# Optimization experiments

Measured on AMD Instinct MI355X. Metric: run time of the kernel, lower is better.

## Reference

```python
import jax, jax.numpy as jnp
import numpy as np

BN_EPS = 1e-5


def three_nn(unknown, known):
    # squared pairwise distances via gemm form: ||u||^2 + ||k||^2 - 2 u.k
    # unknown: (B, n, 3), known: (B, m, 3) -> d: (B, n, m)
    u2 = jnp.sum(unknown * unknown, axis=-1, keepdims=True)          # (B, n, 1)
    k2 = jnp.sum(known * known, axis=-1)[:, None, :]                 # (B, 1, m)
    d = u2 + k2 - 2.0 * jnp.einsum('bnc,bmc->bnm', unknown, known)   # (B, n, m)
    neg_d, idx = jax.lax.top_k(-d, 3)                                # 3 smallest
    return -neg_d, idx                                               # (B,n,3), (B,n,3) int32


def three_interpolate(known_feats, idx, weight):
    # known_feats: (B, C, m), idx/weight: (B, n, 3) -> (B, C, n)
    g = jnp.take_along_axis(known_feats[:, :, None, :], idx[:, None, :, :], axis=3)  # (B,C,n,3)
    return jnp.sum(g * weight[:, None, :, :], axis=3)


def conv1x1(x, W, b):
    # x: (B, C_in, N), W: (C_out, C_in), b: (C_out,)
    return jnp.einsum('oc,bcn->bon', W, x) + b[None, :, None]


def batchnorm(x, gamma, beta):
    # training-mode BN over (B, N) per channel, biased variance
    mean = jnp.mean(x, axis=(0, 2), keepdims=True)
    var = jnp.mean((x - mean) ** 2, axis=(0, 2), keepdims=True)
    xn = (x - mean) * jax.lax.rsqrt(var + BN_EPS)
    return xn * gamma[None, :, None] + beta[None, :, None]


def setup_inputs() -> dict:
    key = jax.random.key(0)
    ks = jax.random.split(key, 16)
    B, n, m = 16, 4096, 1024
    C1, C2, C = 128, 256, 256  # in_channels, known feat channels (=mlp[0]), mlp width
    inp = {
        'unknown': jax.random.normal(ks[0], (B, n, 3), jnp.float32),
        'known': jax.random.normal(ks[1], (B, m, 3), jnp.float32),
        'unknow_feats': jax.random.normal(ks[2], (B, C1, n), jnp.float32),
        'known_feats': jax.random.normal(ks[3], (B, C2, m), jnp.float32),
        # mlp_unknow: Conv1d(C1->C) + BN (no relu)
        'Wu': jax.random.normal(ks[4], (C, C1), jnp.float32) * (1.0 / np.sqrt(C1)),
        'bu': jnp.zeros((C,), jnp.float32),
        'gu': jnp.ones((C,), jnp.float32),
        'betau': jnp.zeros((C,), jnp.float32),
        # mlp_convs[0]: Conv1d(C->C) + BN + relu
        'W1': jax.random.normal(ks[5], (C, C), jnp.float32) * (1.0 / np.sqrt(C)),
        'b1': jnp.zeros((C,), jnp.float32),
        'g1': jnp.ones((C,), jnp.float32),
        'beta1': jnp.zeros((C,), jnp.float32),
        # mlp_convs[1]: Conv1d(C->C) + BN + relu
        'W2': jax.random.normal(ks[6], (C, C), jnp.float32) * (1.0 / np.sqrt(C)),
        'b2': jnp.zeros((C,), jnp.float32),
        'g2': jnp.ones((C,), jnp.float32),
        'beta2': jnp.zeros((C,), jnp.float32),
    }
    return inp


def reference(unknown, known, unknow_feats, known_feats,
              Wu, bu, gu, betau, W1, b1, g1, beta1, W2, b2, g2, beta2):
    dist, idx = three_nn(unknown, known)            # squared dists (B,n,3)
    dist_recip = 1.0 / (dist + 1e-8)
    norm = jnp.sum(dist_recip, axis=2, keepdims=True)
    weight = dist_recip / norm
    interpolated = three_interpolate(known_feats, idx, weight)   # (B, 256, n)

    skip = batchnorm(conv1x1(unknow_feats, Wu, bu), gu, betau)   # (B, 256, n)
    x = interpolated + skip
    x = jax.nn.relu(batchnorm(conv1x1(x, W1, b1), g1, beta1))
    x = jax.nn.relu(batchnorm(conv1x1(x, W2, b2), g2, beta2))
    return x
```

## Files before the change

kernel.cpp:

```cpp
#include <hip/hip_runtime.h>
#include <hip/hip_bf16.h>
#include <cstddef>
#include <cstdint>

#define BATCH 16
#define NPTS  4096
#define MPTS  1024
#define PTOT  65536
#define C1    128
#define C2    256

typedef short bf16x8 __attribute__((ext_vector_type(8)));
typedef float f32x4  __attribute__((ext_vector_type(4)));
typedef unsigned int u32x4 __attribute__((ext_vector_type(4)));

static __device__ __forceinline__ float bf2f(unsigned int u16) {
    union { unsigned int i; float f; } v; v.i = u16 << 16; return v.f;
}
static __device__ __forceinline__ unsigned short f2bf(float f) {
    union { float f; unsigned int i; } v; v.f = f;
    unsigned int u = v.i;
    return (unsigned short)((u + 0x7FFFu + ((u >> 16) & 1u)) >> 16);
}

static __device__ __forceinline__ void st_wt_b128(void* p, u32x4 v) {
    asm volatile("global_store_dwordx4 %0, %1, off sc0 sc1" :: "v"(p), "v"(v) : "memory");
}
static __device__ __forceinline__ void st_wt_f128(void* p, f32x4 v) {
    asm volatile("global_store_dwordx4 %0, %1, off sc0 sc1" :: "v"(p), "v"(v) : "memory");
}
static __device__ __forceinline__ void st_wt_b32(void* p, unsigned v) {
    asm volatile("global_store_dword %0, %1, off sc0 sc1" :: "v"(p), "v"(v) : "memory");
}
static __device__ __forceinline__ void st_wt_b16(void* p, unsigned v) {
    asm volatile("global_store_short %0, %1, off sc0 sc1" :: "v"(p), "v"(v) : "memory");
}

template <int SWZ>
__global__ void k_transpose(const float* __restrict__ in, unsigned short* __restrict__ out,
                            int C, int N) {
    __shared__ float tile[64][65];
    int b  = blockIdx.z;
    int n0 = blockIdx.x * 64;
    int c0 = blockIdx.y * 64;
    const float* src = in + (size_t)b * C * N;
    unsigned short* dst = out + (size_t)b * N * C;
    int t  = threadIdx.x;
    int t4 = t >> 6;
    int tn = t & 63;
#pragma unroll
    for (int i = 0; i < 16; ++i) {
        int cc = i * 4 + t4;
        tile[cc][tn] = src[(size_t)(c0 + cc) * N + n0 + tn];
    }
    __syncthreads();
#pragma unroll
    for (int i = 0; i < 16; ++i) {
        int nn = i * 4 + t4;
        int p  = n0 + nn;
        int c  = c0 + tn;
        size_t off;
        if (SWZ) off = (size_t)p * C + (size_t)((((c >> 3) ^ (p & 7)) << 3) + (c & 7));
        else     off = (size_t)p * C + c;
        st_wt_b16(dst + off, (unsigned)f2bf(tile[tn][nn]));
    }
}

__global__ void k_cvt_pack(const float* __restrict__ in, unsigned short* __restrict__ out, int K) {
    int tid = blockIdx.x * 256 + threadIdx.x;
    if (tid >= 256 * K) return;
    int ch = tid / K, k = tid % K;
    int ks = k >> 5, lhi = (k >> 3) & 3, e = k & 7;
    int wv = ch >> 6, i = (ch >> 4) & 3, llo = ch & 15;
    int lane = lhi * 16 + llo;
    st_wt_b16(out + ((size_t)((ks * 16 + wv * 4 + i) * 64 + lane)) * 8 + e,
              (unsigned)f2bf(in[tid]));
}

static __device__ __forceinline__ bool nn_less(float da, int ia, float db, int ib) {
    return (da < db) || (da == db && ia < ib);
}

__global__ void k_three_nn(const float* __restrict__ unknown, const float* __restrict__ known,
                           int* __restrict__ idx_out, float* __restrict__ w_out) {
    __shared__ float4 kpt[MPTS + 4];
    int t  = threadIdx.x;
    int p0 = blockIdx.x * 64;
    int b  = p0 >> 12;
    const float* kb = known + (size_t)b * MPTS * 3;
    for (int i = t; i < MPTS; i += 256) {
        float x = kb[i * 3 + 0], y = kb[i * 3 + 1], z = kb[i * 3 + 2];
        float dd = __fadd_rn(__fadd_rn(__fmul_rn(x, x), __fmul_rn(y, y)), __fmul_rn(z, z));
        float4 v; v.x = x; v.y = y; v.z = z; v.w = dd;
        kpt[i + (i >> 8)] = v;
    }
    __syncthreads();

    int q = t & 3;
    int p = p0 + (t >> 2);
    const float* up = unknown + (size_t)p * 3;
    float ux = up[0], uy = up[1], uz = up[2];
    float u2 = __fadd_rn(__fadd_rn(__fmul_rn(ux, ux), __fmul_rn(uy, uy)), __fmul_rn(uz, uz));

    float d0 = INFINITY, d1 = INFINITY, d2 = INFINITY;
    int   i0 = 0, i1 = 0, i2 = 0;
    int base = q * 257;
#pragma unroll 4
    for (int it = 0; it < 256; ++it) {
        float4 kp = kpt[base + it];
        float dot = __fadd_rn(__fadd_rn(__fmul_rn(ux, kp.x), __fmul_rn(uy, kp.y)),
                              __fmul_rn(uz, kp.z));
        float d = __fsub_rn(__fadd_rn(u2, kp.w), __fmul_rn(2.0f, dot));
        int k = q * 256 + it;
        if (d < d0)      { d2 = d1; i2 = i1; d1 = d0; i1 = i0; d0 = d; i0 = k; }
        else if (d < d1) { d2 = d1; i2 = i1; d1 = d;  i1 = k; }
        else if (d < d2) { d2 = d;  i2 = k; }
    }

#pragma unroll
    for (int m = 1; m <= 2; m <<= 1) {
        float e0 = __shfl_xor(d0, m, 64), e1 = __shfl_xor(d1, m, 64), e2 = __shfl_xor(d2, m, 64);
        int   j0 = __shfl_xor(i0, m, 64), j1 = __shfl_xor(i1, m, 64), j2 = __shfl_xor(i2, m, 64);
        float a0 = d0, a1 = d1, a2 = d2; int x0 = i0, x1 = i1, x2 = i2;
        float b0 = e0, b1 = e1, b2 = e2; int y0 = j0, y1 = j1, y2 = j2;
        bool tk = nn_less(a0, x0, b0, y0);
        d0 = tk ? a0 : b0; i0 = tk ? x0 : y0;
        float na0 = tk ? a1 : a0; int nx0 = tk ? x1 : x0;
        float na1 = tk ? a2 : a1; int nx1 = tk ? x2 : x1;
        float nb0 = tk ? b0 : b1; int ny0 = tk ? y0 : y1;
        float nb1 = tk ? b1 : b2; int ny1 = tk ? y1 : y2;
        tk = nn_less(na0, nx0, nb0, ny0);
        d1 = tk ? na0 : nb0; i1 = tk ? nx0 : ny0;
        float ma0 = tk ? na1 : na0; int mx0 = tk ? nx1 : nx0;
        float mb0 = tk ? nb0 : nb1; int my0 = tk ? ny0 : ny1;
        tk = nn_less(ma0, mx0, mb0, my0);
        d2 = tk ? ma0 : mb0; i2 = tk ? mx0 : my0;
    }

    if (q == 0) {
        float r0 = 1.0f / (d0 + 1e-8f), r1 = 1.0f / (d1 + 1e-8f), r2 = 1.0f / (d2 + 1e-8f);
        float norm = r0 + r1 + r2;
        size_t pg = (size_t)p;
        st_wt_b32(idx_out + pg * 3 + 0, (unsigned)i0);
        st_wt_b32(idx_out + pg * 3 + 1, (unsigned)i1);
        st_wt_b32(idx_out + pg * 3 + 2, (unsigned)i2);
        union { float f; unsigned u; } w0v, w1v, w2v;
        w0v.f = r0 / norm; w1v.f = r1 / norm; w2v.f = r2 / norm;
        st_wt_b32(w_out + pg * 3 + 0, w0v.u);
        st_wt_b32(w_out + pg * 3 + 1, w1v.u);
        st_wt_b32(w_out + pg * 3 + 2, w2v.u);
    }
}

template <int K, int MODE>
__global__ __launch_bounds__(256, 4) void k_gemm(
        const unsigned short* __restrict__ Wp,
        const unsigned short* __restrict__ X,
        const float* __restrict__ Xf,
        const float* __restrict__ bias,
        const float* __restrict__ aff_a,
        const float* __restrict__ aff_c,
        unsigned short* __restrict__ Y,
        float* __restrict__ partial) {
    constexpr int NK = K / 32;
    constexpr int TB = 16 * K * 2;
    __shared__ char smem[8192];

    const int t    = threadIdx.x;
    const int p0   = blockIdx.x * 16;
    const int wv   = t >> 6;
    const int lane = t & 63;
    const int lhi  = lane >> 4, llo = lane & 15;

    if (MODE == 0) {
        const char* src = (const char*)(X + (size_t)p0 * K);
        constexpr int ITERS = TB / (256 * 16);
#pragma unroll
        for (int i = 0; i < ITERS; ++i) {
            int off = (i * 256 + t) * 16;
            __builtin_amdgcn_global_load_lds(
                (const __attribute__((address_space(1))) unsigned int*)(src + off),
                (__attribute__((address_space(3))) unsigned int*)(smem + off),
                16, 0, 0);
        }
    } else if (MODE == 1) {
        constexpr int CPR = K / 8;
#pragma unroll
        for (int i = 0; i < (16 * CPR) / 256; ++i) {
            int f   = i * 256 + t;
            int row = f / CPR, qp = f % CPR;
            int col = qp ^ (row & 7);
            uint4 v = *(const uint4*)(X + (size_t)(p0 + row) * K + qp * 8);
            unsigned int w[4] = {v.x, v.y, v.z, v.w};
            float4 a0 = *(const float4*)(aff_a + col * 8);
            float4 a1 = *(const float4*)(aff_a + col * 8 + 4);
            float4 cc0 = *(const float4*)(aff_c + col * 8);
            float4 cc1 = *(const float4*)(aff_c + col * 8 + 4);
            float aa[8] = {a0.x, a0.y, a0.z, a0.w, a1.x, a1.y, a1.z, a1.w};
            float cc[8] = {cc0.x, cc0.y, cc0.z, cc0.w, cc1.x, cc1.y, cc1.z, cc1.w};
#pragma unroll
            for (int q2 = 0; q2 < 4; ++q2) {
                float lo = fmaxf(bf2f(w[q2] & 0xffff) * aa[q2 * 2]     + cc[q2 * 2],     0.0f);
                float hi = fmaxf(bf2f(w[q2] >> 16)    * aa[q2 * 2 + 1] + cc[q2 * 2 + 1], 0.0f);
                w[q2] = (unsigned int)f2bf(lo) | ((unsigned int)f2bf(hi) << 16);
            }
            uint4 o; o.x = w[0]; o.y = w[1]; o.z = w[2]; o.w = w[3];
            *(uint4*)(smem + row * (K * 2) + qp * 16) = o;
        }
    } else {
        int c    = t >> 1;
        int half = (t & 1) * 8;
        int b    = p0 >> 12;
        const float* src = Xf + ((size_t)b * C1 + c) * NPTS + (p0 & 4095) + half;
        float4 v0 = *(const float4*)(src);
        float4 v1 = *(const float4*)(src + 4);
        float fv[8] = {v0.x, v0.y, v0.z, v0.w, v1.x, v1.y, v1.z, v1.w};
#pragma unroll
        for (int e = 0; e < 8; ++e) {
            int p = half + e;
            *(unsigned short*)(smem + p * (K * 2) +
                               ((((c >> 3) ^ (p & 7)) << 4) + (c & 7) * 2)) = f2bf(fv[e]);
        }
    }

    const unsigned short* wbase = Wp + ((size_t)(wv * 256) + lane) * 8;
    bf16x8 wA[4], wB[4];
#pragma unroll
    for (int i = 0; i < 4; ++i)
        wA[i] = *(const bf16x8*)(wbase + i * 512);

    __syncthreads();

    f32x4 acc[4];
#pragma unroll
    for (int i = 0; i < 4; ++i) acc[i] = (f32x4){0.f, 0.f, 0.f, 0.f};

#pragma unroll
    for (int ks = 0; ks < NK; ks += 2) {
#pragma unroll
        for (int i = 0; i < 4; ++i)
            wB[i] = *(const bf16x8*)(wbase + (size_t)(ks + 1) * 8192 + i * 512);
        {
            int cp = (ks * 4 + lhi) ^ (llo & 7);
            bf16x8 bb = *(const bf16x8*)(smem + llo * (K * 2) + cp * 16);
#pragma unroll
            for (int i = 0; i < 4; ++i)
                acc[i] = __builtin_amdgcn_mfma_f32_16x16x32_bf16(wA[i], bb, acc[i], 0, 0, 0);
        }
        if (ks + 2 < NK) {
#pragma unroll
            for (int i = 0; i < 4; ++i)
                wA[i] = *(const bf16x8*)(wbase + (size_t)(ks + 2) * 8192 + i * 512);
        }
        {
            int cp = ((ks + 1) * 4 + lhi) ^ (llo & 7);
            bf16x8 bb = *(const bf16x8*)(smem + llo * (K * 2) + cp * 16);
#pragma unroll
            for (int i = 0; i < 4; ++i)
                acc[i] = __builtin_amdgcn_mfma_f32_16x16x32_bf16(wB[i], bb, acc[i], 0, 0, 0);
        }
    }

    __syncthreads();
#pragma unroll
    for (int i = 0; i < 4; ++i) {
        int cbase = wv * 64 + i * 16 + lhi * 4;
        float4 bv = *(const float4*)(bias + cbase);
        int c8 = cbase >> 3, hf = lhi & 1;
        int row = llo;
        float y0 = acc[i][0] + bv.x;
        float y1 = acc[i][1] + bv.y;
        float y2 = acc[i][2] + bv.z;
        float y3 = acc[i][3] + bv.w;
        float s0 = y0, q0 = y0 * y0;
        float s1 = y1, q1 = y1 * y1;
        float s2 = y2, q2 = y2 * y2;
        float s3 = y3, q3 = y3 * y3;
        unsigned int lo = (unsigned int)f2bf(y0) | ((unsigned int)f2bf(y1) << 16);
        unsigned int hi = (unsigned int)f2bf(y2) | ((unsigned int)f2bf(y3) << 16);
        uint2 o; o.x = lo; o.y = hi;
        *(uint2*)(smem + row * 512 + ((c8 ^ (row & 7)) << 4) + hf * 8) = o;
#pragma unroll
        for (int m = 1; m <= 8; m <<= 1) {
            s0 += __shfl_xor(s0, m, 64); q0 += __shfl_xor(q0, m, 64);
            s1 += __shfl_xor(s1, m, 64); q1 += __shfl_xor(q1, m, 64);
            s2 += __shfl_xor(s2, m, 64); q2 += __shfl_xor(q2, m, 64);
            s3 += __shfl_xor(s3, m, 64); q3 += __shfl_xor(q3, m, 64);
        }
        if (llo == 0) {
            f32x4 sv = {s0, s1, s2, s3};
            f32x4 qv = {q0, q1, q2, q3};
            st_wt_f128(partial + (size_t)blockIdx.x * 512 + cbase, sv);
            st_wt_f128(partial + (size_t)blockIdx.x * 512 + 256 + cbase, qv);
        }
    }
    __syncthreads();
    {
        const char* ysrc = smem + t * 16;
        char* ydst = (char*)(Y + (size_t)p0 * 256) + t * 16;
        u32x4 v0 = *(const u32x4*)(ysrc);
        u32x4 v1 = *(const u32x4*)(ysrc + 4096);
        st_wt_b128(ydst, v0);
        st_wt_b128(ydst + 4096, v1);
    }
}

__global__ void k_red1(const float* __restrict__ partial, float* __restrict__ partA) {
    int t = threadIdx.x, g = blockIdx.x;
    float s = 0.f, q = 0.f;
#pragma unroll 8
    for (int i = 0; i < 64; ++i) {
        const float* pp = partial + (size_t)(g * 64 + i) * 512;
        s += pp[t]; q += pp[256 + t];
    }
    union { float f; unsigned u; } sv, qv; sv.f = s; qv.f = q;
    st_wt_b32(partA + g * 512 + t, sv.u);
    st_wt_b32(partA + g * 512 + 256 + t, qv.u);
}

__global__ void k_finalize(const float* __restrict__ partA, const float* __restrict__ gamma,
                           const float* __restrict__ beta, float* __restrict__ aff_a,
                           float* __restrict__ aff_c) {
    int c = threadIdx.x;
    float s = 0.f, q = 0.f;
#pragma unroll 8
    for (int i = 0; i < 64; ++i) { s += partA[i * 512 + c]; q += partA[i * 512 + 256 + c]; }
    float mean = s * (1.0f / PTOT);
    float var  = fmaxf(q * (1.0f / PTOT) - mean * mean, 0.0f);
    float a    = gamma[c] / sqrtf(var + 1e-5f);
    union { float f; unsigned u; } av, cv;
    av.f = a; cv.f = beta[c] - mean * a;
    st_wt_b32(aff_a + c, av.u);
    st_wt_b32(aff_c + c, cv.u);
}

__global__ void k_build_x(const unsigned short* __restrict__ y0, const unsigned short* __restrict__ kfT,
                          const int* __restrict__ idx, const float* __restrict__ wgt,
                          const float* __restrict__ aff_a, const float* __restrict__ aff_c,
                          unsigned short* __restrict__ X) {
    int t   = threadIdx.x;
    int p   = blockIdx.x * 8 + (t >> 5);
    int col = t & 31;
    int c0  = col * 8;
    int b   = p >> 12;
    int pos = col ^ (p & 7);
    int i0 = idx[p * 3 + 0], i1 = idx[p * 3 + 1], i2 = idx[p * 3 + 2];
    float w0 = wgt[p * 3 + 0], w1 = wgt[p * 3 + 1], w2 = wgt[p * 3 + 2];
    const size_t kb = (size_t)b * MPTS * C2;
    uint4 v0 = *(const uint4*)(kfT + kb + (size_t)i0 * C2 + c0);
    uint4 v1 = *(const uint4*)(kfT + kb + (size_t)i1 * C2 + c0);
    uint4 v2 = *(const uint4*)(kfT + kb + (size_t)i2 * C2 + c0);
    uint4 vy = *(const uint4*)(y0 + (size_t)p * C2 + pos * 8);
    const unsigned int* u0 = (const unsigned int*)&v0;
    const unsigned int* u1 = (const unsigned int*)&v1;
    const unsigned int* u2 = (const unsigned int*)&v2;
    const unsigned int* uy = (const unsigned int*)&vy;
    unsigned int r[4];
#pragma unroll
    for (int q = 0; q < 4; ++q) {
        int c = c0 + q * 2;
        float lo = w0 * bf2f(u0[q] & 0xffff) + w1 * bf2f(u1[q] & 0xffff) + w2 * bf2f(u2[q] & 0xffff)
                 + bf2f(uy[q] & 0xffff) * aff_a[c] + aff_c[c];
        float hi = w0 * bf2f(u0[q] >> 16) + w1 * bf2f(u1[q] >> 16) + w2 * bf2f(u2[q] >> 16)
                 + bf2f(uy[q] >> 16) * aff_a[c + 1] + aff_c[c + 1];
        r[q] = (unsigned int)f2bf(lo) | ((unsigned int)f2bf(hi) << 16);
    }
    uint4 vout; vout.x = r[0]; vout.y = r[1]; vout.z = r[2]; vout.w = r[3];
    *(uint4*)(X + (size_t)p * C2 + pos * 8) = vout;
}

__global__ void k_final(const unsigned short* __restrict__ Y2, const float* __restrict__ aff_a,
                        const float* __restrict__ aff_c, float* __restrict__ out) {
    __shared__ float tile[64][65];
    int p0 = blockIdx.x * 64;
    int c0 = blockIdx.y * 64;
    int t  = threadIdx.x;
    int t4 = t >> 6, t64 = t & 63;
#pragma unroll
    for (int i = 0; i < 16; ++i) {
        int r = i * 4 + t4;
        int p = p0 + r;
        int c = c0 + t64;
        float v = bf2f(Y2[(size_t)p * 256 + (((c >> 3) ^ (p & 7)) << 3) + (c & 7)])
                  * aff_a[c] + aff_c[c];
        tile[t64][r] = fmaxf(v, 0.0f);
    }
    __syncthreads();
    int b   = p0 >> 12;
    int pin = p0 & 4095;
#pragma unroll
    for (int i = 0; i < 16; ++i) {
        int cc = i * 4 + t4;
        __builtin_nontemporal_store(tile[cc][t64],
            out + ((size_t)b * 256 + c0 + cc) * 4096 + pin + t64);
    }
}

extern "C" void kernel_launch(void* const* d_in, const int* in_sizes, int n_in,
                              void* d_out, int out_size, void* d_ws, size_t ws_size,
                              hipStream_t stream) {
    const float* unknown = (const float*)d_in[0];
    const float* known   = (const float*)d_in[1];
    const float* ufeat   = (const float*)d_in[2];
    const float* kfeat   = (const float*)d_in[3];
    const float* Wu      = (const float*)d_in[4];
    const float* bu      = (const float*)d_in[5];
    const float* gu      = (const float*)d_in[6];
    const float* betau   = (const float*)d_in[7];
    const float* W1      = (const float*)d_in[8];
    const float* b1      = (const float*)d_in[9];
    const float* g1      = (const float*)d_in[10];
    const float* beta1   = (const float*)d_in[11];
    const float* W2      = (const float*)d_in[12];
    const float* b2      = (const float*)d_in[13];
    const float* g2      = (const float*)d_in[14];
    const float* beta2   = (const float*)d_in[15];
    float* out = (float*)d_out;

    char* ws = (char*)d_ws;
    unsigned short* reg0 = (unsigned short*)ws;
    unsigned short* ybuf = (unsigned short*)(ws + ((size_t)32 << 20));
    unsigned short* kfT  = (unsigned short*)(ws + ((size_t)64 << 20));
    unsigned short* Wub  = (unsigned short*)(ws + ((size_t)72 << 20));
    unsigned short* W1b  = Wub + 256 * 128;
    unsigned short* W2b  = W1b + 256 * 256;
    int*   idxb = (int*)(W2b + 256 * 256);
    float* wgtb = (float*)(idxb + (size_t)PTOT * 3);
    float* affa0 = wgtb + (size_t)PTOT * 3;
    float* affc0 = affa0 + 256;
    float* affa1 = affc0 + 256;
    float* affc1 = affa1 + 256;
    float* affa2 = affc1 + 256;
    float* affc2 = affa2 + 256;
    float* partA = affc2 + 256;
    float* part0  = (float*)(ws + ((size_t)16 << 20));
    float* part12 = (float*)(ws + ((size_t)64 << 20));
    if (ws_size < ((size_t)75 << 20)) return;

    k_transpose<0><<<dim3(MPTS / 64, C2 / 64, BATCH), 256, 0, stream>>>(kfeat, kfT, C2, MPTS);
    k_cvt_pack<<<128, 256, 0, stream>>>(Wu, Wub, 128);
    k_cvt_pack<<<256, 256, 0, stream>>>(W1, W1b, 256);
    k_cvt_pack<<<256, 256, 0, stream>>>(W2, W2b, 256);

    k_three_nn<<<PTOT / 64, 256, 0, stream>>>(unknown, known, idxb, wgtb);

    k_gemm<C1, 2><<<PTOT / 16, 256, 0, stream>>>(Wub, nullptr, ufeat, bu, nullptr, nullptr,
                                                 ybuf, part0);
    k_red1<<<64, 256, 0, stream>>>(part0, partA);
    k_finalize<<<1, 256, 0, stream>>>(partA, gu, betau, affa0, affc0);

    k_build_x<<<PTOT / 8, 256, 0, stream>>>(ybuf, kfT, idxb, wgtb, affa0, affc0, reg0);

    k_gemm<C2, 0><<<PTOT / 16, 256, 0, stream>>>(W1b, reg0, nullptr, b1, nullptr, nullptr,
                                                 ybuf, part12);
    k_red1<<<64, 256, 0, stream>>>(part12, partA);
    k_finalize<<<1, 256, 0, stream>>>(partA, g1, beta1, affa1, affc1);

    k_gemm<C2, 1><<<PTOT / 16, 256, 0, stream>>>(W2b, ybuf, nullptr, b2, affa1, affc1,
                                                 reg0, part12);
    k_red1<<<64, 256, 0, stream>>>(part12, partA);
    k_finalize<<<1, 256, 0, stream>>>(partA, g2, beta2, affa2, affc2);

    k_final<<<dim3(PTOT / 64, 4), 256, 0, stream>>>(reg0, affa2, affc2, out);

    (void)in_sizes; (void)n_in; (void)out_size;
}
```

Before: 220.8 us.

## Fuse interpolation build into first MLP GEMM and split three_nn scan wider

The separate k_build_x pass that gathered three neighbour features, applied the skip-branch BN affine and wrote a bf16 X buffer is folded into the GEMM prologue as a new MODE 3. The first MLP GEMM now builds its input tile directly in shared memory, which removes one full write and read of the 65536x256 activation buffer. The three_nn kernel now splits each point's scan across 8 lanes instead of 4, with 32 points per block and one more shuffle-merge round, for more parallelism per point. Partial-sum buffers are relocated, including reuse of the output buffer as scratch. This relies on the output being fully rewritten later by k_final.

Result: faster. 211.0 us (-4.4%).

```diff
diff --git a/kernel.cpp b/kernel.cpp
--- a/kernel.cpp
+++ b/kernel.cpp
@@ -83,42 +83,42 @@
 
 __global__ void k_three_nn(const float* __restrict__ unknown, const float* __restrict__ known,
                            int* __restrict__ idx_out, float* __restrict__ w_out) {
-    __shared__ float4 kpt[MPTS + 4];
+    __shared__ float4 kpt[MPTS + 8];
     int t  = threadIdx.x;
-    int p0 = blockIdx.x * 64;
+    int p0 = blockIdx.x * 32;
     int b  = p0 >> 12;
     const float* kb = known + (size_t)b * MPTS * 3;
     for (int i = t; i < MPTS; i += 256) {
         float x = kb[i * 3 + 0], y = kb[i * 3 + 1], z = kb[i * 3 + 2];
         float dd = __fadd_rn(__fadd_rn(__fmul_rn(x, x), __fmul_rn(y, y)), __fmul_rn(z, z));
         float4 v; v.x = x; v.y = y; v.z = z; v.w = dd;
-        kpt[i + (i >> 8)] = v;
-    }
-    __syncthreads();
-
-    int q = t & 3;
-    int p = p0 + (t >> 2);
+        kpt[i + (i >> 7)] = v;
+    }
+    __syncthreads();
+
+    int q = t & 7;
+    int p = p0 + (t >> 3);
     const float* up = unknown + (size_t)p * 3;
     float ux = up[0], uy = up[1], uz = up[2];
     float u2 = __fadd_rn(__fadd_rn(__fmul_rn(ux, ux), __fmul_rn(uy, uy)), __fmul_rn(uz, uz));
 
     float d0 = INFINITY, d1 = INFINITY, d2 = INFINITY;
     int   i0 = 0, i1 = 0, i2 = 0;
-    int base = q * 257;
+    int base = q * 129;
 #pragma unroll 4
-    for (int it = 0; it < 256; ++it) {
+    for (int it = 0; it < 128; ++it) {
         float4 kp = kpt[base + it];
         float dot = __fadd_rn(__fadd_rn(__fmul_rn(ux, kp.x), __fmul_rn(uy, kp.y)),
                               __fmul_rn(uz, kp.z));
         float d = __fsub_rn(__fadd_rn(u2, kp.w), __fmul_rn(2.0f, dot));
-        int k = q * 256 + it;
+        int k = q * 128 + it;
         if (d < d0)      { d2 = d1; i2 = i1; d1 = d0; i1 = i0; d0 = d; i0 = k; }
         else if (d < d1) { d2 = d1; i2 = i1; d1 = d;  i1 = k; }
         else if (d < d2) { d2 = d;  i2 = k; }
     }
 
 #pragma unroll
-    for (int m = 1; m <= 2; m <<= 1) {
+    for (int m = 1; m <= 4; m <<= 1) {
         float e0 = __shfl_xor(d0, m, 64), e1 = __shfl_xor(d1, m, 64), e2 = __shfl_xor(d2, m, 64);
         int   j0 = __shfl_xor(i0, m, 64), j1 = __shfl_xor(i1, m, 64), j2 = __shfl_xor(i2, m, 64);
         float a0 = d0, a1 = d1, a2 = d2; int x0 = i0, x1 = i1, x2 = i2;
@@ -157,6 +157,9 @@
         const unsigned short* __restrict__ Wp,
         const unsigned short* __restrict__ X,
         const float* __restrict__ Xf,
+        const unsigned short* __restrict__ kfT,
+        const int* __restrict__ idx,
+        const float* __restrict__ wgt,
         const float* __restrict__ bias,
         const float* __restrict__ aff_a,
         const float* __restrict__ aff_c,
@@ -207,7 +210,7 @@
             uint4 o; o.x = w[0]; o.y = w[1]; o.z = w[2]; o.w = w[3];
             *(uint4*)(smem + row * (K * 2) + qp * 16) = o;
         }
-    } else {
+    } else if (MODE == 2) {
         int c    = t >> 1;
         int half = (t & 1) * 8;
         int b    = p0 >> 12;
@@ -220,6 +223,43 @@
             int p = half + e;
             *(unsigned short*)(smem + p * (K * 2) +
                                ((((c >> 3) ^ (p & 7)) << 4) + (c & 7) * 2)) = f2bf(fv[e]);
+        }
+    } else {
+        int pj  = t >> 4;
+        int sub = t & 15;
+        int p   = p0 + pj;
+        int b   = p >> 12;
+        int i0 = idx[p * 3 + 0], i1 = idx[p * 3 + 1], i2 = idx[p * 3 + 2];
+        float w0 = wgt[p * 3 + 0], w1 = wgt[p * 3 + 1], w2 = wgt[p * 3 + 2];
+        const unsigned short* kb = kfT + (size_t)b * MPTS * C2;
+#pragma unroll
+        for (int cc2 = 0; cc2 < 2; ++cc2) {
+            int cc = sub * 2 + cc2;
+            int cbase = cc * 8;
+            u32x4 v0 = *(const u32x4*)(kb + (size_t)i0 * C2 + cbase);
+            u32x4 v1 = *(const u32x4*)(kb + (size_t)i1 * C2 + cbase);
+            u32x4 v2 = *(const u32x4*)(kb + (size_t)i2 * C2 + cbase);
+            int pos = cc ^ (p & 7);
+            u32x4 vy = *(const u32x4*)(X + (size_t)p * C2 + pos * 8);
+            float4 a0 = *(const float4*)(aff_a + cbase);
+            float4 a1 = *(const float4*)(aff_a + cbase + 4);
+            float4 c0f = *(const float4*)(aff_c + cbase);
+            float4 c1f = *(const float4*)(aff_c + cbase + 4);
+            float aa[8] = {a0.x, a0.y, a0.z, a0.w, a1.x, a1.y, a1.z, a1.w};
+            float cf[8] = {c0f.x, c0f.y, c0f.z, c0f.w, c1f.x, c1f.y, c1f.z, c1f.w};
+            unsigned r[4];
+#pragma unroll
+            for (int qq = 0; qq < 4; ++qq) {
+                float lo = w0 * bf2f(v0[qq] & 0xffff) + w1 * bf2f(v1[qq] & 0xffff)
+                         + w2 * bf2f(v2[qq] & 0xffff)
+                         + bf2f(vy[qq] & 0xffff) * aa[qq * 2] + cf[qq * 2];
+                float hi = w0 * bf2f(v0[qq] >> 16) + w1 * bf2f(v1[qq] >> 16)
+                         + w2 * bf2f(v2[qq] >> 16)
+                         + bf2f(vy[qq] >> 16) * aa[qq * 2 + 1] + cf[qq * 2 + 1];
+                r[qq] = (unsigned)f2bf(lo) | ((unsigned)f2bf(hi) << 16);
+            }
+            u32x4 vo; vo.x = r[0]; vo.y = r[1]; vo.z = r[2]; vo.w = r[3];
+            *(u32x4*)(smem + pj * 512 + pos * 16) = vo;
         }
     }
 
@@ -332,41 +372,6 @@
     av.f = a; cv.f = beta[c] - mean * a;
     st_wt_b32(aff_a + c, av.u);
     st_wt_b32(aff_c + c, cv.u);
-}
-
-__global__ void k_build_x(const unsigned short* __restrict__ y0, const unsigned short* __restrict__ kfT,
-                          const int* __restrict__ idx, const float* __restrict__ wgt,
-                          const float* __restrict__ aff_a, const float* __restrict__ aff_c,
-                          unsigned short* __restrict__ X) {
-    int t   = threadIdx.x;
-    int p   = blockIdx.x * 8 + (t >> 5);
-    int col = t & 31;
-    int c0  = col * 8;
-    int b   = p >> 12;
-    int pos = col ^ (p & 7);
-    int i0 = idx[p * 3 + 0], i1 = idx[p * 3 + 1], i2 = idx[p * 3 + 2];
-    float w0 = wgt[p * 3 + 0], w1 = wgt[p * 3 + 1], w2 = wgt[p * 3 + 2];
-    const size_t kb = (size_t)b * MPTS * C2;
-    uint4 v0 = *(const uint4*)(kfT + kb + (size_t)i0 * C2 + c0);
-    uint4 v1 = *(const uint4*)(kfT + kb + (size_t)i1 * C2 + c0);
-    uint4 v2 = *(const uint4*)(kfT + kb + (size_t)i2 * C2 + c0);
-    uint4 vy = *(const uint4*)(y0 + (size_t)p * C2 + pos * 8);
-    const unsigned int* u0 = (const unsigned int*)&v0;
-    const unsigned int* u1 = (const unsigned int*)&v1;
-    const unsigned int* u2 = (const unsigned int*)&v2;
-    const unsigned int* uy = (const unsigned int*)&vy;
-    unsigned int r[4];
-#pragma unroll
-    for (int q = 0; q < 4; ++q) {
-        int c = c0 + q * 2;
-        float lo = w0 * bf2f(u0[q] & 0xffff) + w1 * bf2f(u1[q] & 0xffff) + w2 * bf2f(u2[q] & 0xffff)
-                 + bf2f(uy[q] & 0xffff) * aff_a[c] + aff_c[c];
-        float hi = w0 * bf2f(u0[q] >> 16) + w1 * bf2f(u1[q] >> 16) + w2 * bf2f(u2[q] >> 16)
-                 + bf2f(uy[q] >> 16) * aff_a[c + 1] + aff_c[c + 1];
-        r[q] = (unsigned int)f2bf(lo) | ((unsigned int)f2bf(hi) << 16);
-    }
-    uint4 vout; vout.x = r[0]; vout.y = r[1]; vout.z = r[2]; vout.w = r[3];
-    *(uint4*)(X + (size_t)p * C2 + pos * 8) = vout;
 }
 
 __global__ void k_final(const unsigned short* __restrict__ Y2, const float* __restrict__ aff_a,
@@ -433,8 +438,8 @@
     float* affa2 = affc1 + 256;
     float* affc2 = affa2 + 256;
     float* partA = affc2 + 256;
-    float* part0  = (float*)(ws + ((size_t)16 << 20));
-    float* part12 = (float*)(ws + ((size_t)64 << 20));
+    float* part0  = (float*)ws;
+    float* partD  = (float*)d_out;
     if (ws_size < ((size_t)75 << 20)) return;
 
     k_transpose<0><<<dim3(MPTS / 64, C2 / 64, BATCH), 256, 0, stream>>>(kfeat, kfT, C2, MPTS);
@@ -442,26 +447,24 @@
     k_cvt_pack<<<256, 256, 0, stream>>>(W1, W1b, 256);
     k_cvt_pack<<<256, 256, 0, stream>>>(W2, W2b, 256);
 
-    k_three_nn<<<PTOT / 64, 256, 0, stream>>>(unknown, known, idxb, wgtb);
-
-    k_gemm<C1, 2><<<PTOT / 16, 256, 0, stream>>>(Wub, nullptr, ufeat, bu, nullptr, nullptr,
-                                                 ybuf, part0);
+    k_three_nn<<<PTOT / 32, 256, 0, stream>>>(unknown, known, idxb, wgtb);
+
+    k_gemm<C1, 2><<<PTOT / 16, 256, 0, stream>>>(Wub, nullptr, ufeat, nullptr, nullptr, nullptr,
+                                                 bu, nullptr, nullptr, ybuf, part0);
     k_red1<<<64, 256, 0, stream>>>(part0, partA);
     k_finalize<<<1, 256, 0, stream>>>(partA, gu, betau, affa0, affc0);
 
-    k_build_x<<<PTOT / 8, 256, 0, stream>>>(ybuf, kfT, idxb, wgtb, affa0, affc0, reg0);
-
-    k_gemm<C2, 0><<<PTOT / 16, 256, 0, stream>>>(W1b, reg0, nullptr, b1, nullptr, nullptr,
-                                                 ybuf, part12);
-    k_red1<<<64, 256, 0, stream>>>(part12, partA);
+    k_gemm<C2, 3><<<PTOT / 16, 256, 0, stream>>>(W1b, ybuf, nullptr, kfT, idxb, wgtb,
+                                                 b1, affa0, affc0, reg0, partD);
+    k_red1<<<64, 256, 0, stream>>>(partD, partA);
     k_finalize<<<1, 256, 0, stream>>>(partA, g1, beta1, affa1, affc1);
 
-    k_gemm<C2, 1><<<PTOT / 16, 256, 0, stream>>>(W2b, ybuf, nullptr, b2, affa1, affc1,
-                                                 reg0, part12);
-    k_red1<<<64, 256, 0, stream>>>(part12, partA);
+    k_gemm<C2, 1><<<PTOT / 16, 256, 0, stream>>>(W2b, reg0, nullptr, nullptr, nullptr, nullptr,
+                                                 b2, affa1, affc1, ybuf, partD);
+    k_red1<<<64, 256, 0, stream>>>(partD, partA);
     k_finalize<<<1, 256, 0, stream>>>(partA, g2, beta2, affa2, affc2);
 
-    k_final<<<dim3(PTOT / 64, 4), 256, 0, stream>>>(reg0, affa2, affc2, out);
+    k_final<<<dim3(PTOT / 64, 4), 256, 0, stream>>>(ybuf, affa2, affc2, out);
 
     (void)in_sizes; (void)n_in; (void)out_size;
 }
```
